# Performance work log

Measured on AMD Instinct MI355X. Metric: run time of the kernel, lower is better.

## Reference

```python
import jax, jax.numpy as jnp
import numpy as np

D_MODEL = 512
N_HEADS = 8
N_KV_HEADS = 2
HEAD_DIM = 64
PITCH_VOCAB = 128


def setup_inputs() -> dict:
    key = jax.random.key(0)
    ks = jax.random.split(key, 6)
    B, T, P = 2, 256, 12
    s = lambda fan_in: 1.0 / np.sqrt(fan_in)
    hidden_states = jax.random.normal(ks[0], (B, T, P, D_MODEL), dtype=jnp.float32)
    Wq = jax.random.normal(ks[1], (D_MODEL, N_HEADS * HEAD_DIM), dtype=jnp.float32) * s(D_MODEL)
    Wk = jax.random.normal(ks[2], (D_MODEL, N_KV_HEADS * HEAD_DIM), dtype=jnp.float32) * s(D_MODEL)
    Wv = jax.random.normal(ks[3], (D_MODEL, N_KV_HEADS * HEAD_DIM), dtype=jnp.float32) * s(D_MODEL)
    Wo = jax.random.normal(ks[4], (N_HEADS * HEAD_DIM, D_MODEL), dtype=jnp.float32) * s(N_HEADS * HEAD_DIM)
    pitch_table = jax.random.normal(ks[5], (PITCH_VOCAB, HEAD_DIM), dtype=jnp.float32)
    return {"hidden_states": hidden_states, "Wq": Wq, "Wk": Wk, "Wv": Wv, "Wo": Wo, "pitch_table": pitch_table}


def reference(hidden_states, Wq, Wk, Wv, Wo, pitch_table):
    B, T, P, C = hidden_states.shape
    H, Hkv, d = N_HEADS, N_KV_HEADS, HEAD_DIM
    rep = H // Hkv

    q = (hidden_states @ Wq).reshape(B, T, P, H, d)
    k = (hidden_states @ Wk).reshape(B, T, P, Hkv, d)
    v = (hidden_states @ Wv).reshape(B, T, P, Hkv, d)

    # GQA repeat_kv: (B,T,P,Hkv,d) -> (B,T,P,H,d)
    k = jnp.repeat(k, rep, axis=3)
    v = jnp.repeat(v, rep, axis=3)

    # additive pitch bias on q and k
    pitch_emb = pitch_table[jnp.arange(P)]  # (P, d)
    bias = pitch_emb[None, None, :, None, :]
    q = q + bias
    k = k + bias

    # flatten (T,P) -> S and move heads forward: (B,H,S,d)
    S = T * P
    q = q.transpose(0, 3, 1, 2, 4).reshape(B, H, S, d)
    k = k.transpose(0, 3, 1, 2, 4).reshape(B, H, S, d)
    v = v.transpose(0, 3, 1, 2, 4).reshape(B, H, S, d)

    scale = 1.0 / jnp.sqrt(jnp.asarray(d, dtype=q.dtype))
    attn = jax.nn.softmax(jnp.einsum('bhqd,bhkd->bhqk', q, k) * scale, axis=-1)
    out = jnp.einsum('bhqk,bhkd->bhqd', attn, v)  # (B,H,S,d)

    out = out.reshape(B, H, T, P, d).transpose(0, 2, 3, 1, 4).reshape(B, T, P, H * d)
    return out @ Wo
```

## Files before the change

kernel.cpp:

```cpp
#include <hip/hip_runtime.h>
#include <hip/hip_fp16.h>

#define B_   2
#define T_   256
#define P_   12
#define C_   512
#define H_   8
#define HKV_ 2
#define D_   64
#define S_   (T_ * P_)
#define M_   (B_ * S_)
#define NQKV 768

typedef _Float16 half8_t __attribute__((ext_vector_type(8)));
typedef _Float16 half4_t __attribute__((ext_vector_type(4)));
typedef _Float16 half2_t __attribute__((ext_vector_type(2)));
typedef float    float4_t __attribute__((ext_vector_type(4)));

#if __has_builtin(__builtin_amdgcn_exp2f)
#define EXP2(x) __builtin_amdgcn_exp2f(x)
#else
#define EXP2(x) __expf((x) * 0.69314718f)
#endif

#define SOFT_SHIFT 20.0f
#define SOFT_CLAMP2 15.5f
#define QSCALE (0.125f * 1.44269504f)

__global__ __launch_bounds__(256) void prep_kernel(
    const float* __restrict__ hs,
    const float* __restrict__ Wq, const float* __restrict__ Wk,
    const float* __restrict__ Wv, const float* __restrict__ Wo,
    _Float16* __restrict__ hs16,
    _Float16* __restrict__ wcatT,
    _Float16* __restrict__ woT)
{
    const int blk = blockIdx.x;
    const int tid = threadIdx.x;

    if (blk < 160) {
        __shared__ __attribute__((aligned(16))) _Float16 Ts[64][72];
        int t, K;
        const float* src; int srcN, col0; _Float16* dst;
        if (blk < 96) { t = blk; K = 512; dst = wcatT;
            int nt = t / 8;
            int kt = t % 8;
            int n0 = nt * 64, k0 = kt * 64;
            if (n0 < 512)      { src = Wq; srcN = 512; col0 = n0; }
            else if (n0 < 640) { src = Wk; srcN = 128; col0 = n0 - 512; }
            else               { src = Wv; srcN = 128; col0 = n0 - 640; }
#pragma unroll
            for (int i = 0; i < 4; ++i) {
                int row = i * 16 + (tid >> 4);
                int cg  = tid & 15;
                float4_t v = *(const float4_t*)(src + (size_t)(k0 + row) * srcN + col0 + cg * 4);
                Ts[cg * 4 + 0][row] = (_Float16)v[0];
                Ts[cg * 4 + 1][row] = (_Float16)v[1];
                Ts[cg * 4 + 2][row] = (_Float16)v[2];
                Ts[cg * 4 + 3][row] = (_Float16)v[3];
            }
            __syncthreads();
#pragma unroll
            for (int i = 0; i < 2; ++i) {
                int seg = i * 256 + tid;
                int row = seg >> 3, s = seg & 7;
                *(half8_t*)(dst + (size_t)(n0 + row) * K + k0 + s * 8) =
                    *(const half8_t*)&Ts[row][s * 8];
            }
        } else { t = blk - 96; K = 512; dst = woT;
            int nt = t / 8, kt = t % 8;
            int n0 = nt * 64, k0 = kt * 64;
#pragma unroll
            for (int i = 0; i < 4; ++i) {
                int row = i * 16 + (tid >> 4);
                int cg  = tid & 15;
                float4_t v = *(const float4_t*)(Wo + (size_t)(k0 + row) * 512 + n0 + cg * 4);
                Ts[cg * 4 + 0][row] = (_Float16)v[0];
                Ts[cg * 4 + 1][row] = (_Float16)v[1];
                Ts[cg * 4 + 2][row] = (_Float16)v[2];
                Ts[cg * 4 + 3][row] = (_Float16)v[3];
            }
            __syncthreads();
#pragma unroll
            for (int i = 0; i < 2; ++i) {
                int seg = i * 256 + tid;
                int row = seg >> 3, s = seg & 7;
                *(half8_t*)(dst + (size_t)(n0 + row) * K + k0 + s * 8) =
                    *(const half8_t*)&Ts[row][s * 8];
            }
        }
    } else {
        int base = (blk - 160) * 4096;
#pragma unroll
        for (int i = 0; i < 16; ++i) {
            int f4 = base + i * 256 + tid;
            float4_t v = *(const float4_t*)(hs + (size_t)f4 * 4);
            half4_t hv;
            hv[0] = (_Float16)v[0]; hv[1] = (_Float16)v[1];
            hv[2] = (_Float16)v[2]; hv[3] = (_Float16)v[3];
            *(half4_t*)(hs16 + (size_t)f4 * 4) = hv;
        }
    }
}

__global__ __launch_bounds__(256) void qkv_kernel(
    const _Float16* __restrict__ A,
    const _Float16* __restrict__ WT,
    const float* __restrict__ pitch,
    _Float16* __restrict__ qb,
    _Float16* __restrict__ kb,
    _Float16* __restrict__ vb)
{
    const int m0   = blockIdx.x * 64;
    const int n0   = blockIdx.y * 64;
    const int tid  = threadIdx.x;
    const int wave = tid >> 6;
    const int lane = tid & 63;
    const int ln   = lane & 15;
    const int quad = lane >> 4;

    __shared__ __attribute__((aligned(16))) _Float16 As[64][72];
    __shared__ __attribute__((aligned(16))) _Float16 Bs[64][72];

    float4_t acc[4];
#pragma unroll
    for (int nt = 0; nt < 4; ++nt) acc[nt] = (float4_t){0.f, 0.f, 0.f, 0.f};

    const int srow = tid >> 3;
    const int ss   = tid & 7;

    half8_t ar[2], br[2];
#pragma unroll
    for (int i = 0; i < 2; ++i) {
        int row = i * 32 + srow;
        ar[i] = *(const half8_t*)&A [(size_t)(m0 + row) * 512 + ss * 8];
        br[i] = *(const half8_t*)&WT[(size_t)(n0 + row) * 512 + ss * 8];
    }

    for (int k0 = 0; k0 < 512; k0 += 64) {
        __syncthreads();
#pragma unroll
        for (int i = 0; i < 2; ++i) {
            int row = i * 32 + srow;
            *(half8_t*)&As[row][ss * 8] = ar[i];
            *(half8_t*)&Bs[row][ss * 8] = br[i];
        }
        __syncthreads();

        if (k0 + 64 < 512) {
#pragma unroll
            for (int i = 0; i < 2; ++i) {
                int row = i * 32 + srow;
                ar[i] = *(const half8_t*)&A [(size_t)(m0 + row) * 512 + k0 + 64 + ss * 8];
                br[i] = *(const half8_t*)&WT[(size_t)(n0 + row) * 512 + k0 + 64 + ss * 8];
            }
        }

#pragma unroll
        for (int ks = 0; ks < 2; ++ks) {
            half8_t afrag = *(const half8_t*)&As[wave * 16 + ln][ks * 32 + quad * 8];
#pragma unroll
            for (int nt = 0; nt < 4; ++nt) {
                half8_t bfrag = *(const half8_t*)&Bs[nt * 16 + ln][ks * 32 + quad * 8];
                acc[nt] = __builtin_amdgcn_mfma_f32_16x16x32_f16(afrag, bfrag, acc[nt], 0, 0, 0);
            }
        }
    }

    const int bb      = m0 / S_;
    const int s00     = m0 - bb * S_;
    const int sl_base = wave * 16 + quad * 4;
    const int s_base  = s00 + sl_base;
    const int p_base  = s_base % P_;

    if (n0 < 512) {
        const int h = n0 >> 6;
#pragma unroll
        for (int r = 0; r < 4; ++r) {
            int p = p_base + r; if (p >= P_) p -= P_;
            const float* pr = pitch + p * 64;
            size_t rowb = ((size_t)(bb * H_ + h) * S_ + s_base + r) * 64;
#pragma unroll
            for (int nt = 0; nt < 4; ++nt) {
                int dd = nt * 16 + ln;
                float v = (acc[nt][r] + pr[dd]) * QSCALE;
                qb[rowb + dd] = (_Float16)v;
            }
        }
    } else if (n0 < 640) {
        const int h = (n0 - 512) >> 6;
#pragma unroll
        for (int r = 0; r < 4; ++r) {
            int p = p_base + r; if (p >= P_) p -= P_;
            const float* pr = pitch + p * 64;
            size_t rowb = ((size_t)(bb * HKV_ + h) * S_ + s_base + r) * 64;
#pragma unroll
            for (int nt = 0; nt < 4; ++nt) {
                int dd = nt * 16 + ln;
                kb[rowb + dd] = (_Float16)(acc[nt][r] + pr[dd]);
            }
        }
    } else {
        const int h = (n0 - 640) >> 6;
        __syncthreads();
#pragma unroll
        for (int nt = 0; nt < 4; ++nt)
#pragma unroll
            for (int r = 0; r < 4; ++r)
                As[nt * 16 + ln][sl_base + r] = (_Float16)acc[nt][r];
        __syncthreads();
        const int rw = tid >> 2;
        const int c0 = (tid & 3) * 16;
        _Float16* dst = vb + ((size_t)(bb * HKV_ + h) * 64 + rw) * S_ + s00 + c0;
        *(half8_t*)dst       = *(const half8_t*)&As[rw][c0];
        *(half8_t*)(dst + 8) = *(const half8_t*)&As[rw][c0 + 8];
    }
}

__global__ __launch_bounds__(512) void attn_kernel(
    const _Float16* __restrict__ qbuf,
    const _Float16* __restrict__ kbuf,
    const _Float16* __restrict__ vtb,
    _Float16* __restrict__ ob)
{
    const int qblk = blockIdx.x;
    const int bh   = blockIdx.y;
    const int b    = bh >> 3;
    const int h    = bh & 7;
    const int hkv  = h >> 2;
    const int tid  = threadIdx.x;
    const int w    = tid >> 6;
    const int lane = tid & 63;
    const int ln   = lane & 15;
    const int quad = lane >> 4;

    const _Float16* Q  = qbuf + ((size_t)(b * H_ + h)) * S_ * 64;
    const _Float16* K  = kbuf + ((size_t)(b * HKV_ + hkv)) * S_ * 64;
    const _Float16* Vt = vtb  + ((size_t)(b * HKV_ + hkv)) * 64 * S_;

    __shared__ __attribute__((aligned(16))) _Float16 Ks[128][80];
    __shared__ __attribute__((aligned(16))) _Float16 VT[2][64][80];
    __shared__ __attribute__((aligned(16))) _Float16 Ps[8][16][40];

    const int qbase = qblk * 64 + (w & 3) * 16;
    const int kk0   = (w >> 2) * 32;

    half8_t qfrag[2];
#pragma unroll
    for (int ks = 0; ks < 2; ++ks)
        qfrag[ks] = *(const half8_t*)&Q[(size_t)(qbase + ln) * 64 + ks * 32 + quad * 8];

    float4_t o[4];
#pragma unroll
    for (int nt = 0; nt < 4; ++nt) o[nt] = (float4_t){0.f, 0.f, 0.f, 0.f};
    float lr[4] = {0.f, 0.f, 0.f, 0.f};

    const int j = tid >> 3, s = tid & 7;
    const int r0 = ((j & 1) << 4) | ((j >> 5) << 5) | ((j >> 1) & 15);

    half8_t kr0, kr1, vr0, vr1;
    kr0 = *(const half8_t*)&K[(size_t)j * 64 + s * 8];
    kr1 = *(const half8_t*)&K[(size_t)(64 + j) * 64 + s * 8];
    vr0 = *(const half8_t*)&Vt[(size_t)j * S_ + s * 8];
    vr1 = *(const half8_t*)&Vt[(size_t)j * S_ + 64 + s * 8];

    for (int kt = 0; kt < S_; kt += 128) {
        __syncthreads();
        *(half8_t*)&Ks[r0][s * 8]      = kr0;
        *(half8_t*)&Ks[r0 + 64][s * 8] = kr1;
        *(half8_t*)&VT[0][j][s * 8]    = vr0;
        *(half8_t*)&VT[1][j][s * 8]    = vr1;
        __syncthreads();

        if (kt + 128 < S_) {
            kr0 = *(const half8_t*)&K[(size_t)(kt + 128 + j) * 64 + s * 8];
            kr1 = *(const half8_t*)&K[(size_t)(kt + 128 + 64 + j) * 64 + s * 8];
            vr0 = *(const half8_t*)&Vt[(size_t)j * S_ + kt + 128 + s * 8];
            vr1 = *(const half8_t*)&Vt[(size_t)j * S_ + kt + 128 + 64 + s * 8];
        }

#pragma unroll
        for (int h2 = 0; h2 < 2; ++h2) {
            const int kb = h2 * 64 + kk0;

            float4_t sf[2];
            __builtin_amdgcn_s_setprio(1);
#pragma unroll
            for (int c = 0; c < 2; ++c) {
                sf[c] = (float4_t){-SOFT_SHIFT, -SOFT_SHIFT, -SOFT_SHIFT, -SOFT_SHIFT};
#pragma unroll
                for (int ks = 0; ks < 2; ++ks) {
                    half8_t kf = *(const half8_t*)&Ks[kb + c * 16 + ln][ks * 32 + quad * 8];
                    sf[c] = __builtin_amdgcn_mfma_f32_16x16x32_f16(qfrag[ks], kf, sf[c], 0, 0, 0);
                }
            }
            __builtin_amdgcn_s_setprio(0);

#pragma unroll
            for (int rr = 0; rr < 4; ++rr) {
                float p0 = EXP2(fminf(sf[0][rr], SOFT_CLAMP2));
                float p1 = EXP2(fminf(sf[1][rr], SOFT_CLAMP2));
                lr[rr] += p0 + p1;
                half2_t w2; w2[0] = (_Float16)p0; w2[1] = (_Float16)p1;
                *(half2_t*)&Ps[w][quad * 4 + rr][2 * ln] = w2;
            }

            half8_t pf = *(const half8_t*)&Ps[w][ln][quad * 8];
            __builtin_amdgcn_s_setprio(1);
#pragma unroll
            for (int nt = 0; nt < 4; ++nt) {
                half8_t vf = *(const half8_t*)&VT[h2][nt * 16 + ln][kk0 + quad * 8];
                o[nt] = __builtin_amdgcn_mfma_f32_16x16x32_f16(pf, vf, o[nt], 0, 0, 0);
            }
            __builtin_amdgcn_s_setprio(0);
        }
    }

    __syncthreads();
    if (w >= 4) {
        float* od = (float*)&Ks[0][0] + (w - 4) * 1280;
#pragma unroll
        for (int nt = 0; nt < 4; ++nt)
            *(float4_t*)&od[lane * 20 + nt * 4] = o[nt];
        float* ld = (float*)&Ps[0][0][0] + (w - 4) * 256;
        *(float4_t*)&ld[lane * 4] = (float4_t){lr[0], lr[1], lr[2], lr[3]};
    }
    __syncthreads();
    if (w < 4) {
        const float* os = (const float*)&Ks[0][0] + w * 1280;
        const float* ls = (const float*)&Ps[0][0][0] + w * 256;
        float4_t ls4 = *(const float4_t*)&ls[lane * 4];
        float4_t os4[4];
#pragma unroll
        for (int nt = 0; nt < 4; ++nt)
            os4[nt] = *(const float4_t*)&os[lane * 20 + nt * 4];
#pragma unroll
        for (int rr = 0; rr < 4; ++rr) {
            float l = lr[rr] + ls4[rr];
            l += __shfl_xor(l, 1);
            l += __shfl_xor(l, 2);
            l += __shfl_xor(l, 4);
            l += __shfl_xor(l, 8);
            float inv = 1.0f / l;
            int qg = qbase + quad * 4 + rr;
            size_t base = ((size_t)(b * S_ + qg)) * 512 + h * 64;
#pragma unroll
            for (int nt = 0; nt < 4; ++nt) {
                float vsum = o[nt][rr] + os4[nt][rr];
                ob[base + nt * 16 + ln] = (_Float16)(vsum * inv);
            }
        }
    }
}

__global__ __launch_bounds__(256) void proj_out_kernel(
    const _Float16* __restrict__ A,
    const _Float16* __restrict__ WT,
    float* __restrict__ outp)
{
    const int m0   = blockIdx.x * 64;
    const int n0   = blockIdx.y * 64;
    const int tid  = threadIdx.x;
    const int wave = tid >> 6;
    const int lane = tid & 63;
    const int ln   = lane & 15;
    const int quad = lane >> 4;

    __shared__ __attribute__((aligned(16))) _Float16 As[64][72];
    __shared__ __attribute__((aligned(16))) _Float16 Bs[64][72];

    float4_t acc[4];
#pragma unroll
    for (int nt = 0; nt < 4; ++nt) acc[nt] = (float4_t){0.f, 0.f, 0.f, 0.f};

    const int srow = tid >> 3;
    const int ss   = tid & 7;

    half8_t ar[2], br[2];
#pragma unroll
    for (int i = 0; i < 2; ++i) {
        int row = i * 32 + srow;
        ar[i] = *(const half8_t*)&A [(size_t)(m0 + row) * 512 + ss * 8];
        br[i] = *(const half8_t*)&WT[(size_t)(n0 + row) * 512 + ss * 8];
    }

    for (int k0 = 0; k0 < 512; k0 += 64) {
        __syncthreads();
#pragma unroll
        for (int i = 0; i < 2; ++i) {
            int row = i * 32 + srow;
            *(half8_t*)&As[row][ss * 8] = ar[i];
            *(half8_t*)&Bs[row][ss * 8] = br[i];
        }
        __syncthreads();

        if (k0 + 64 < 512) {
#pragma unroll
            for (int i = 0; i < 2; ++i) {
                int row = i * 32 + srow;
                ar[i] = *(const half8_t*)&A [(size_t)(m0 + row) * 512 + k0 + 64 + ss * 8];
                br[i] = *(const half8_t*)&WT[(size_t)(n0 + row) * 512 + k0 + 64 + ss * 8];
            }
        }

#pragma unroll
        for (int ks = 0; ks < 2; ++ks) {
            half8_t afrag = *(const half8_t*)&As[wave * 16 + ln][ks * 32 + quad * 8];
#pragma unroll
            for (int nt = 0; nt < 4; ++nt) {
                half8_t bfrag = *(const half8_t*)&Bs[nt * 16 + ln][ks * 32 + quad * 8];
                acc[nt] = __builtin_amdgcn_mfma_f32_16x16x32_f16(afrag, bfrag, acc[nt], 0, 0, 0);
            }
        }
    }

#pragma unroll
    for (int nt = 0; nt < 4; ++nt) {
        int n = n0 + nt * 16 + ln;
#pragma unroll
        for (int r = 0; r < 4; ++r) {
            int m = m0 + wave * 16 + quad * 4 + r;
            outp[(size_t)m * 512 + n] = acc[nt][r];
        }
    }
}

extern "C" void kernel_launch(void* const* d_in, const int* in_sizes, int n_in,
                              void* d_out, int out_size, void* d_ws, size_t ws_size,
                              hipStream_t stream) {
    const float* hs    = (const float*)d_in[0];
    const float* Wq    = (const float*)d_in[1];
    const float* Wk    = (const float*)d_in[2];
    const float* Wv    = (const float*)d_in[3];
    const float* Wo    = (const float*)d_in[4];
    const float* pitch = (const float*)d_in[5];
    float* out = (float*)d_out;

    _Float16* hs16  = (_Float16*)d_ws;
    _Float16* o_buf = hs16;
    _Float16* q_buf = hs16 + (size_t)M_ * 512;
    _Float16* k_buf = q_buf + (size_t)B_ * H_ * S_ * 64;
    _Float16* v_buf = k_buf + (size_t)B_ * HKV_ * S_ * 64;
    _Float16* wcatT = v_buf + (size_t)B_ * HKV_ * S_ * 64;
    _Float16* woT   = wcatT + (size_t)NQKV * 512;

    prep_kernel<<<352, 256, 0, stream>>>(hs, Wq, Wk, Wv, Wo, hs16, wcatT, woT);
    qkv_kernel<<<dim3(M_ / 64, NQKV / 64), 256, 0, stream>>>(hs16, wcatT, pitch, q_buf, k_buf, v_buf);
    attn_kernel<<<dim3(S_ / 64, B_ * H_), 512, 0, stream>>>(q_buf, k_buf, v_buf, o_buf);
    proj_out_kernel<<<dim3(M_ / 64, 8), 256, 0, stream>>>(o_buf, woT, out);
}
```

Baseline: 157.0 us.

## Load K/V tiles directly to LDS and repartition waves across queries and keys

```diff
diff --git a/kernel.cpp b/kernel.cpp
--- a/kernel.cpp
+++ b/kernel.cpp
@@ -26,6 +26,11 @@
 #define SOFT_SHIFT 20.0f
 #define SOFT_CLAMP2 15.5f
 #define QSCALE (0.125f * 1.44269504f)
+
+#define GLDS16(gp, lp)                                                          \
+    __builtin_amdgcn_global_load_lds(                                           \
+        (const __attribute__((address_space(1))) void*)(gp),                    \
+        (__attribute__((address_space(3))) void*)(lp), 16, 0, 0)
 
 __global__ __launch_bounds__(256) void prep_kernel(
     const float* __restrict__ hs,
@@ -238,116 +243,163 @@
     const _Float16* K  = kbuf + ((size_t)(b * HKV_ + hkv)) * S_ * 64;
     const _Float16* Vt = vtb  + ((size_t)(b * HKV_ + hkv)) * 64 * S_;
 
-    __shared__ __attribute__((aligned(16))) _Float16 Ks[128][80];
-    __shared__ __attribute__((aligned(16))) _Float16 VT[2][64][80];
-    __shared__ __attribute__((aligned(16))) _Float16 Ps[8][16][40];
-
-    const int qbase = qblk * 64 + (w & 3) * 16;
-    const int kk0   = (w >> 2) * 32;
-
-    half8_t qfrag[2];
-#pragma unroll
-    for (int ks = 0; ks < 2; ++ks)
-        qfrag[ks] = *(const half8_t*)&Q[(size_t)(qbase + ln) * 64 + ks * 32 + quad * 8];
-
-    float4_t o[4];
-#pragma unroll
-    for (int nt = 0; nt < 4; ++nt) o[nt] = (float4_t){0.f, 0.f, 0.f, 0.f};
-    float lr[4] = {0.f, 0.f, 0.f, 0.f};
-
-    const int j = tid >> 3, s = tid & 7;
-    const int r0 = ((j & 1) << 4) | ((j >> 5) << 5) | ((j >> 1) & 15);
-
-    half8_t kr0, kr1, vr0, vr1;
-    kr0 = *(const half8_t*)&K[(size_t)j * 64 + s * 8];
-    kr1 = *(const half8_t*)&K[(size_t)(64 + j) * 64 + s * 8];
-    vr0 = *(const half8_t*)&Vt[(size_t)j * S_ + s * 8];
-    vr1 = *(const half8_t*)&Vt[(size_t)j * S_ + 64 + s * 8];
+    __shared__ __attribute__((aligned(16))) _Float16 smem[8192 + 8192 + 5120];
+    _Float16* Ks = smem;
+    _Float16* VT = smem + 8192;
+    _Float16* Ps = smem + 16384;
+
+    const int qsplit = w & 1;
+    const int ksplit = w >> 1;
+    const int qbase  = qblk * 64 + qsplit * 32;
+    const int kk0    = ksplit * 32;
+
+    half8_t qfrag[2][2];
+#pragma unroll
+    for (int sub = 0; sub < 2; ++sub)
+#pragma unroll
+        for (int ks = 0; ks < 2; ++ks)
+            qfrag[sub][ks] = *(const half8_t*)&Q[(size_t)(qbase + sub * 16 + ln) * 64 + ks * 32 + quad * 8];
+
+    float4_t o[2][4];
+#pragma unroll
+    for (int sub = 0; sub < 2; ++sub)
+#pragma unroll
+        for (int nt = 0; nt < 4; ++nt) o[sub][nt] = (float4_t){0.f, 0.f, 0.f, 0.f};
+    float lr[2][4] = {{0.f,0.f,0.f,0.f},{0.f,0.f,0.f,0.f}};
+
+    const int l3 = lane >> 3, g8 = lane & 7;
+    const int key0 = 32 * (w >> 1) + 2 * l3 + (w & 1);
+    const int kgof0 = key0 * 64 + (g8 ^ l3) * 8;
+    const int kgof1 = kgof0 + 1024;
+    _Float16* ldsK0 = Ks + (w * 16) * 64;
+
+    const int l4 = lane >> 4, g16 = lane & 15;
+    const size_t vgof0 = (size_t)(8 * w + l4) * S_ + (size_t)((g16 ^ l4) * 8);
+    const size_t vgof1 = (size_t)(8 * w + 4 + l4) * S_ + (size_t)((g16 ^ ((4 + l4) & 7)) * 8);
+    _Float16* ldsV0 = VT + (8 * w) * 128;
+
+    const int kxor = (ln & 7) << 3;
 
     for (int kt = 0; kt < S_; kt += 128) {
         __syncthreads();
-        *(half8_t*)&Ks[r0][s * 8]      = kr0;
-        *(half8_t*)&Ks[r0 + 64][s * 8] = kr1;
-        *(half8_t*)&VT[0][j][s * 8]    = vr0;
-        *(half8_t*)&VT[1][j][s * 8]    = vr1;
-        __syncthreads();
-
-        if (kt + 128 < S_) {
-            kr0 = *(const half8_t*)&K[(size_t)(kt + 128 + j) * 64 + s * 8];
-            kr1 = *(const half8_t*)&K[(size_t)(kt + 128 + 64 + j) * 64 + s * 8];
-            vr0 = *(const half8_t*)&Vt[(size_t)j * S_ + kt + 128 + s * 8];
-            vr1 = *(const half8_t*)&Vt[(size_t)j * S_ + kt + 128 + 64 + s * 8];
-        }
-
-#pragma unroll
-        for (int h2 = 0; h2 < 2; ++h2) {
-            const int kb = h2 * 64 + kk0;
-
-            float4_t sf[2];
-            __builtin_amdgcn_s_setprio(1);
+        GLDS16(K + (size_t)kt * 64 + kgof0, ldsK0);
+        GLDS16(K + (size_t)kt * 64 + kgof1, ldsK0 + 512);
+        GLDS16(Vt + kt + vgof0, ldsV0);
+        GLDS16(Vt + kt + vgof1, ldsV0 + 512);
+        asm volatile("s_waitcnt vmcnt(0)" ::: "memory");
+        __syncthreads();
+
+        float4_t sf[2][2];
+#pragma unroll
+        for (int sub = 0; sub < 2; ++sub)
+#pragma unroll
+            for (int c = 0; c < 2; ++c)
+                sf[sub][c] = (float4_t){-SOFT_SHIFT, -SOFT_SHIFT, -SOFT_SHIFT, -SOFT_SHIFT};
+        __builtin_amdgcn_s_setprio(1);
+#pragma unroll
+        for (int ks = 0; ks < 2; ++ks) {
 #pragma unroll
             for (int c = 0; c < 2; ++c) {
-                sf[c] = (float4_t){-SOFT_SHIFT, -SOFT_SHIFT, -SOFT_SHIFT, -SOFT_SHIFT};
-#pragma unroll
-                for (int ks = 0; ks < 2; ++ks) {
-                    half8_t kf = *(const half8_t*)&Ks[kb + c * 16 + ln][ks * 32 + quad * 8];
-                    sf[c] = __builtin_amdgcn_mfma_f32_16x16x32_f16(qfrag[ks], kf, sf[c], 0, 0, 0);
-                }
-            }
-            __builtin_amdgcn_s_setprio(0);
-
+                const int row = kk0 + c * 16 + ln;
+                half8_t kf = *(const half8_t*)&Ks[row * 64 + ((ks * 32 + quad * 8) ^ kxor)];
+                sf[0][c] = __builtin_amdgcn_mfma_f32_16x16x32_f16(qfrag[0][ks], kf, sf[0][c], 0, 0, 0);
+                sf[1][c] = __builtin_amdgcn_mfma_f32_16x16x32_f16(qfrag[1][ks], kf, sf[1][c], 0, 0, 0);
+            }
+        }
+        __builtin_amdgcn_s_setprio(0);
+
+        half8_t pf[2];
+        _Float16* psw = Ps + w * 640;
+#pragma unroll
+        for (int sub = 0; sub < 2; ++sub) {
 #pragma unroll
             for (int rr = 0; rr < 4; ++rr) {
-                float p0 = EXP2(fminf(sf[0][rr], SOFT_CLAMP2));
-                float p1 = EXP2(fminf(sf[1][rr], SOFT_CLAMP2));
-                lr[rr] += p0 + p1;
-                half2_t w2; w2[0] = (_Float16)p0; w2[1] = (_Float16)p1;
-                *(half2_t*)&Ps[w][quad * 4 + rr][2 * ln] = w2;
-            }
-
-            half8_t pf = *(const half8_t*)&Ps[w][ln][quad * 8];
-            __builtin_amdgcn_s_setprio(1);
-#pragma unroll
-            for (int nt = 0; nt < 4; ++nt) {
-                half8_t vf = *(const half8_t*)&VT[h2][nt * 16 + ln][kk0 + quad * 8];
-                o[nt] = __builtin_amdgcn_mfma_f32_16x16x32_f16(pf, vf, o[nt], 0, 0, 0);
-            }
-            __builtin_amdgcn_s_setprio(0);
-        }
-    }
-
-    __syncthreads();
-    if (w >= 4) {
-        float* od = (float*)&Ks[0][0] + (w - 4) * 1280;
-#pragma unroll
-        for (int nt = 0; nt < 4; ++nt)
-            *(float4_t*)&od[lane * 20 + nt * 4] = o[nt];
-        float* ld = (float*)&Ps[0][0][0] + (w - 4) * 256;
-        *(float4_t*)&ld[lane * 4] = (float4_t){lr[0], lr[1], lr[2], lr[3]};
-    }
-    __syncthreads();
-    if (w < 4) {
-        const float* os = (const float*)&Ks[0][0] + w * 1280;
-        const float* ls = (const float*)&Ps[0][0][0] + w * 256;
-        float4_t ls4 = *(const float4_t*)&ls[lane * 4];
-        float4_t os4[4];
-#pragma unroll
-        for (int nt = 0; nt < 4; ++nt)
-            os4[nt] = *(const float4_t*)&os[lane * 20 + nt * 4];
+                float e0 = EXP2(fminf(sf[sub][0][rr], SOFT_CLAMP2));
+                float e1 = EXP2(fminf(sf[sub][1][rr], SOFT_CLAMP2));
+                lr[sub][rr] += e0 + e1;
+                half2_t w2; w2[0] = (_Float16)e0; w2[1] = (_Float16)e1;
+                *(half2_t*)&psw[(quad * 4 + rr) * 40 + 2 * ln] = w2;
+            }
+            pf[sub] = *(const half8_t*)&psw[ln * 40 + quad * 8];
+        }
+
+        __builtin_amdgcn_s_setprio(1);
+#pragma unroll
+        for (int nt = 0; nt < 4; ++nt) {
+            half8_t vf = *(const half8_t*)&VT[(nt * 16 + ln) * 128 + ((kk0 + quad * 8) ^ kxor)];
+            o[0][nt] = __builtin_amdgcn_mfma_f32_16x16x32_f16(pf[0], vf, o[0][nt], 0, 0, 0);
+            o[1][nt] = __builtin_amdgcn_mfma_f32_16x16x32_f16(pf[1], vf, o[1][nt], 0, 0, 0);
+        }
+        __builtin_amdgcn_s_setprio(0);
+    }
+
+#pragma unroll
+    for (int sub = 0; sub < 2; ++sub)
 #pragma unroll
         for (int rr = 0; rr < 4; ++rr) {
-            float l = lr[rr] + ls4[rr];
+            float l = lr[sub][rr];
             l += __shfl_xor(l, 1);
             l += __shfl_xor(l, 2);
             l += __shfl_xor(l, 4);
             l += __shfl_xor(l, 8);
-            float inv = 1.0f / l;
-            int qg = qbase + quad * 4 + rr;
-            size_t base = ((size_t)(b * S_ + qg)) * 512 + h * 64;
-#pragma unroll
-            for (int nt = 0; nt < 4; ++nt) {
-                float vsum = o[nt][rr] + os4[nt][rr];
-                ob[base + nt * 16 + ln] = (_Float16)(vsum * inv);
+            lr[sub][rr] = l;
+        }
+
+    __syncthreads();
+    float* smemF = (float*)smem;
+    float* Lb    = smemF + 8192;
+    if (ln == 0) {
+#pragma unroll
+        for (int sub = 0; sub < 2; ++sub)
+#pragma unroll
+            for (int rr = 0; rr < 4; ++rr)
+                Lb[w * 32 + sub * 16 + quad * 4 + rr] = lr[sub][rr];
+    }
+    if (w >= 4) {
+        float* od = smemF + (w - 4) * 2048;
+#pragma unroll
+        for (int sub = 0; sub < 2; ++sub)
+#pragma unroll
+            for (int nt = 0; nt < 4; ++nt)
+                *(float4_t*)&od[(sub * 4 + nt) * 256 + lane * 4] = o[sub][nt];
+    }
+    __syncthreads();
+    if (w < 4) {
+        const float* os = smemF + w * 2048;
+#pragma unroll
+        for (int sub = 0; sub < 2; ++sub)
+#pragma unroll
+            for (int nt = 0; nt < 4; ++nt)
+                o[sub][nt] += *(const float4_t*)&os[(sub * 4 + nt) * 256 + lane * 4];
+    }
+    __syncthreads();
+    if (w == 2 || w == 3) {
+        float* od = smemF + (w - 2) * 2048;
+#pragma unroll
+        for (int sub = 0; sub < 2; ++sub)
+#pragma unroll
+            for (int nt = 0; nt < 4; ++nt)
+                *(float4_t*)&od[(sub * 4 + nt) * 256 + lane * 4] = o[sub][nt];
+    }
+    __syncthreads();
+    if (w < 2) {
+        const float* os = smemF + w * 2048;
+#pragma unroll
+        for (int sub = 0; sub < 2; ++sub) {
+#pragma unroll
+            for (int rr = 0; rr < 4; ++rr) {
+                int idx = sub * 16 + quad * 4 + rr;
+                float l = Lb[w * 32 + idx] + Lb[(w + 2) * 32 + idx]
+                        + Lb[(w + 4) * 32 + idx] + Lb[(w + 6) * 32 + idx];
+                float inv = 1.0f / l;
+                int qg = qbase + sub * 16 + quad * 4 + rr;
+                size_t base = ((size_t)(b * S_ + qg)) * 512 + h * 64;
+#pragma unroll
+                for (int nt = 0; nt < 4; ++nt) {
+                    float vsum = o[sub][nt][rr]
+                               + os[(sub * 4 + nt) * 256 + lane * 4 + rr];
+                    ob[base + nt * 16 + ln] = (_Float16)(vsum * inv);
+                }
             }
         }
     }
```

Result: slower. 167.5 us (+6.6%).

## Stream GEMM tiles straight to LDS with double buffering and XOR swizzle

Applied to the files above, without the earlier changes.

```diff
diff --git a/kernel.cpp b/kernel.cpp
--- a/kernel.cpp
+++ b/kernel.cpp
@@ -26,6 +26,11 @@
 #define SOFT_SHIFT 20.0f
 #define SOFT_CLAMP2 15.5f
 #define QSCALE (0.125f * 1.44269504f)
+
+#define GLDS16(gp, lp)                                                          \
+    __builtin_amdgcn_global_load_lds(                                           \
+        (const __attribute__((address_space(1))) void*)(gp),                    \
+        (__attribute__((address_space(3))) void*)(lp), 16, 0, 0)
 
 __global__ __launch_bounds__(256) void prep_kernel(
     const float* __restrict__ hs,
@@ -119,53 +124,56 @@
     const int ln   = lane & 15;
     const int quad = lane >> 4;
 
-    __shared__ __attribute__((aligned(16))) _Float16 As[64][72];
-    __shared__ __attribute__((aligned(16))) _Float16 Bs[64][72];
+    __shared__ __attribute__((aligned(16))) _Float16 gs[16384];
 
     float4_t acc[4];
 #pragma unroll
     for (int nt = 0; nt < 4; ++nt) acc[nt] = (float4_t){0.f, 0.f, 0.f, 0.f};
 
-    const int srow = tid >> 3;
-    const int ss   = tid & 7;
-
-    half8_t ar[2], br[2];
-#pragma unroll
-    for (int i = 0; i < 2; ++i) {
-        int row = i * 32 + srow;
-        ar[i] = *(const half8_t*)&A [(size_t)(m0 + row) * 512 + ss * 8];
-        br[i] = *(const half8_t*)&WT[(size_t)(n0 + row) * 512 + ss * 8];
-    }
-
-    for (int k0 = 0; k0 < 512; k0 += 64) {
-        __syncthreads();
-#pragma unroll
-        for (int i = 0; i < 2; ++i) {
-            int row = i * 32 + srow;
-            *(half8_t*)&As[row][ss * 8] = ar[i];
-            *(half8_t*)&Bs[row][ss * 8] = br[i];
-        }
-        __syncthreads();
-
-        if (k0 + 64 < 512) {
-#pragma unroll
-            for (int i = 0; i < 2; ++i) {
-                int row = i * 32 + srow;
-                ar[i] = *(const half8_t*)&A [(size_t)(m0 + row) * 512 + k0 + 64 + ss * 8];
-                br[i] = *(const half8_t*)&WT[(size_t)(n0 + row) * 512 + k0 + 64 + ss * 8];
-            }
-        }
+    const int srow = wave * 8 + (lane >> 3);
+    const int sg   = (lane & 7) ^ (lane >> 3);
+    const _Float16* Asrc = A  + (size_t)(m0 + srow) * 512 + sg * 8;
+    const _Float16* Bsrc = WT + (size_t)(n0 + srow) * 512 + sg * 8;
+    _Float16* const awd = gs + wave * 512;
+    _Float16* const bwd = gs + 8192 + wave * 512;
+
+#define QKV_STAGE(buf, k0)                                        \
+    do {                                                          \
+        GLDS16(Asrc + (k0),         awd + (buf) * 4096);          \
+        GLDS16(Asrc + (k0) + 16384, awd + (buf) * 4096 + 2048);   \
+        GLDS16(Bsrc + (k0),         bwd + (buf) * 4096);          \
+        GLDS16(Bsrc + (k0) + 16384, bwd + (buf) * 4096 + 2048);   \
+    } while (0)
+
+    const int colx = (ln & 7) << 3;
+
+    QKV_STAGE(0, 0);
+    asm volatile("s_waitcnt vmcnt(0)" ::: "memory");
+    __syncthreads();
+
+#pragma unroll
+    for (int kk = 0; kk < 8; ++kk) {
+        const int cur = kk & 1;
+        if (kk < 7) QKV_STAGE(cur ^ 1, (kk + 1) * 64);
 
 #pragma unroll
         for (int ks = 0; ks < 2; ++ks) {
-            half8_t afrag = *(const half8_t*)&As[wave * 16 + ln][ks * 32 + quad * 8];
-#pragma unroll
-            for (int nt = 0; nt < 4; ++nt) {
-                half8_t bfrag = *(const half8_t*)&Bs[nt * 16 + ln][ks * 32 + quad * 8];
+            half8_t afrag = *(const half8_t*)&gs[cur * 4096 +
+                (wave * 16 + ln) * 64 + ((ks * 32 + quad * 8) ^ colx)];
+#pragma unroll
+            for (int nt = 0; nt < 4; ++nt) {
+                half8_t bfrag = *(const half8_t*)&gs[8192 + cur * 4096 +
+                    (nt * 16 + ln) * 64 + ((ks * 32 + quad * 8) ^ colx)];
                 acc[nt] = __builtin_amdgcn_mfma_f32_16x16x32_f16(afrag, bfrag, acc[nt], 0, 0, 0);
             }
         }
-    }
+
+        if (kk < 7) {
+            asm volatile("s_waitcnt vmcnt(0)" ::: "memory");
+            __syncthreads();
+        }
+    }
+#undef QKV_STAGE
 
     const int bb      = m0 / S_;
     const int s00     = m0 - bb * S_;
@@ -207,13 +215,15 @@
         for (int nt = 0; nt < 4; ++nt)
 #pragma unroll
             for (int r = 0; r < 4; ++r)
-                As[nt * 16 + ln][sl_base + r] = (_Float16)acc[nt][r];
+                gs[(nt * 16 + ln) * 64 + ((sl_base + r) ^ ((ln & 7) << 3))] =
+                    (_Float16)acc[nt][r];
         __syncthreads();
         const int rw = tid >> 2;
         const int c0 = (tid & 3) * 16;
+        const int rx = (rw & 7) << 3;
         _Float16* dst = vb + ((size_t)(bb * HKV_ + h) * 64 + rw) * S_ + s00 + c0;
-        *(half8_t*)dst       = *(const half8_t*)&As[rw][c0];
-        *(half8_t*)(dst + 8) = *(const half8_t*)&As[rw][c0 + 8];
+        *(half8_t*)dst       = *(const half8_t*)&gs[rw * 64 + (c0 ^ rx)];
+        *(half8_t*)(dst + 8) = *(const half8_t*)&gs[rw * 64 + ((c0 + 8) ^ rx)];
     }
 }
 
@@ -239,7 +249,7 @@
     const _Float16* Vt = vtb  + ((size_t)(b * HKV_ + hkv)) * 64 * S_;
 
     __shared__ __attribute__((aligned(16))) _Float16 Ks[128][80];
-    __shared__ __attribute__((aligned(16))) _Float16 VT[2][64][80];
+    __shared__ __attribute__((aligned(16))) _Float16 VT[64][136];
     __shared__ __attribute__((aligned(16))) _Float16 Ps[8][16][40];
 
     const int qbase = qblk * 64 + (w & 3) * 16;
@@ -268,8 +278,8 @@
         __syncthreads();
         *(half8_t*)&Ks[r0][s * 8]      = kr0;
         *(half8_t*)&Ks[r0 + 64][s * 8] = kr1;
-        *(half8_t*)&VT[0][j][s * 8]    = vr0;
-        *(half8_t*)&VT[1][j][s * 8]    = vr1;
+        *(half8_t*)&VT[j][s * 8]       = vr0;
+        *(half8_t*)&VT[j][64 + s * 8]  = vr1;
         __syncthreads();
 
         if (kt + 128 < S_) {
@@ -309,7 +319,7 @@
             __builtin_amdgcn_s_setprio(1);
 #pragma unroll
             for (int nt = 0; nt < 4; ++nt) {
-                half8_t vf = *(const half8_t*)&VT[h2][nt * 16 + ln][kk0 + quad * 8];
+                half8_t vf = *(const half8_t*)&VT[nt * 16 + ln][kb + quad * 8];
                 o[nt] = __builtin_amdgcn_mfma_f32_16x16x32_f16(pf, vf, o[nt], 0, 0, 0);
             }
             __builtin_amdgcn_s_setprio(0);
@@ -366,53 +376,56 @@
     const int ln   = lane & 15;
     const int quad = lane >> 4;
 
-    __shared__ __attribute__((aligned(16))) _Float16 As[64][72];
-    __shared__ __attribute__((aligned(16))) _Float16 Bs[64][72];
+    __shared__ __attribute__((aligned(16))) _Float16 gs[16384];
 
     float4_t acc[4];
 #pragma unroll
     for (int nt = 0; nt < 4; ++nt) acc[nt] = (float4_t){0.f, 0.f, 0.f, 0.f};
 
-    const int srow = tid >> 3;
-    const int ss   = tid & 7;
-
-    half8_t ar[2], br[2];
-#pragma unroll
-    for (int i = 0; i < 2; ++i) {
-        int row = i * 32 + srow;
-        ar[i] = *(const half8_t*)&A [(size_t)(m0 + row) * 512 + ss * 8];
-        br[i] = *(const half8_t*)&WT[(size_t)(n0 + row) * 512 + ss * 8];
-    }
-
-    for (int k0 = 0; k0 < 512; k0 += 64) {
-        __syncthreads();
-#pragma unroll
-        for (int i = 0; i < 2; ++i) {
-            int row = i * 32 + srow;
-            *(half8_t*)&As[row][ss * 8] = ar[i];
-            *(half8_t*)&Bs[row][ss * 8] = br[i];
-        }
-        __syncthreads();
-
-        if (k0 + 64 < 512) {
-#pragma unroll
-            for (int i = 0; i < 2; ++i) {
-                int row = i * 32 + srow;
-                ar[i] = *(const half8_t*)&A [(size_t)(m0 + row) * 512 + k0 + 64 + ss * 8];
-                br[i] = *(const half8_t*)&WT[(size_t)(n0 + row) * 512 + k0 + 64 + ss * 8];
-            }
-        }
+    const int srow = wave * 8 + (lane >> 3);
+    const int sg   = (lane & 7) ^ (lane >> 3);
+    const _Float16* Asrc = A  + (size_t)(m0 + srow) * 512 + sg * 8;
+    const _Float16* Bsrc = WT + (size_t)(n0 + srow) * 512 + sg * 8;
+    _Float16* const awd = gs + wave * 512;
+    _Float16* const bwd = gs + 8192 + wave * 512;
+
+#define PRJ_STAGE(buf, k0)                                        \
+    do {                                                          \
+        GLDS16(Asrc + (k0),         awd + (buf) * 4096);          \
+        GLDS16(Asrc + (k0) + 16384, awd + (buf) * 4096 + 2048);   \
+        GLDS16(Bsrc + (k0),         bwd + (buf) * 4096);          \
+        GLDS16(Bsrc + (k0) + 16384, bwd + (buf) * 4096 + 2048);   \
+    } while (0)
+
+    const int colx = (ln & 7) << 3;
+
+    PRJ_STAGE(0, 0);
+    asm volatile("s_waitcnt vmcnt(0)" ::: "memory");
+    __syncthreads();
+
+#pragma unroll
+    for (int kk = 0; kk < 8; ++kk) {
+        const int cur = kk & 1;
+        if (kk < 7) PRJ_STAGE(cur ^ 1, (kk + 1) * 64);
 
 #pragma unroll
         for (int ks = 0; ks < 2; ++ks) {
-            half8_t afrag = *(const half8_t*)&As[wave * 16 + ln][ks * 32 + quad * 8];
-#pragma unroll
-            for (int nt = 0; nt < 4; ++nt) {
-                half8_t bfrag = *(const half8_t*)&Bs[nt * 16 + ln][ks * 32 + quad * 8];
+            half8_t afrag = *(const half8_t*)&gs[cur * 4096 +
+                (wave * 16 + ln) * 64 + ((ks * 32 + quad * 8) ^ colx)];
+#pragma unroll
+            for (int nt = 0; nt < 4; ++nt) {
+                half8_t bfrag = *(const half8_t*)&gs[8192 + cur * 4096 +
+                    (nt * 16 + ln) * 64 + ((ks * 32 + quad * 8) ^ colx)];
                 acc[nt] = __builtin_amdgcn_mfma_f32_16x16x32_f16(afrag, bfrag, acc[nt], 0, 0, 0);
             }
         }
-    }
+
+        if (kk < 7) {
+            asm volatile("s_waitcnt vmcnt(0)" ::: "memory");
+            __syncthreads();
+        }
+    }
+#undef PRJ_STAGE
 
 #pragma unroll
     for (int nt = 0; nt < 4; ++nt) {
```

New measurement: 162.3 us. 3.4% more time.
